# Kernel optimization log

Measured on AMD Instinct MI355X. Metric: run time of the kernel, lower is better.

The kernel has to match this reference:

```python
import jax, jax.numpy as jnp
import numpy as np

EPS = 1e-6

def _elu_feature_map(x):
    # fast_transformers default feature map: elu(x) + 1 (always positive)
    return jax.nn.elu(x) + 1.0

def setup_inputs() -> dict:
    key = jax.random.key(0)
    ks = jax.random.split(key, 7)
    f, n, c, hid = 1024, 64, 256, 1024
    s = 1.0 / np.sqrt(c)
    return {
        "x": jax.random.normal(ks[0], (f, n, c), dtype=jnp.float32),
        "Wq": jax.random.normal(ks[1], (c, hid), dtype=jnp.float32) * s,
        "bq": jax.random.normal(ks[2], (hid,), dtype=jnp.float32) * 0.01,
        "Wk": jax.random.normal(ks[3], (c, hid), dtype=jnp.float32) * s,
        "bk": jax.random.normal(ks[4], (hid,), dtype=jnp.float32) * 0.01,
        "Wv": jax.random.normal(ks[5], (c, hid), dtype=jnp.float32) * s,
        "bv": jax.random.normal(ks[6], (hid,), dtype=jnp.float32) * 0.01,
    }

def reference(x, Wq, bq, Wk, bk, Wv, bv):
    heads = 8
    f, n, c = x.shape
    xt = jnp.transpose(x, (1, 0, 2))  # (n, f, c): joints as batch, frames as sequence
    q = xt @ Wq + bq  # (n, f, hid)
    k = xt @ Wk + bk
    v = xt @ Wv + bv
    hid = q.shape[-1]
    d = hid // heads
    q = q.reshape(n, f, heads, d)
    k = k.reshape(n, f, heads, d)
    v = v.reshape(n, f, heads, d)
    # Linear (kernelized) attention, non-causal (FullMask + full LengthMask)
    Q = _elu_feature_map(q)  # (n, f, h, d)
    K = _elu_feature_map(k)
    KV = jnp.einsum('nshd,nshm->nhmd', K, v)          # (n, h, d_v, d_k)
    Ksum = K.sum(axis=1)                               # (n, h, d_k)
    Z = 1.0 / (jnp.einsum('nlhd,nhd->nlh', Q, Ksum) + EPS)  # (n, f, h)
    out = jnp.einsum('nlhd,nhmd,nlh->nlhm', Q, KV, Z)  # (n, f, h, d_v)
    # faithful to rearrange('f n h c -> n f (h c)') applied to (n, f, h, d):
    # swaps first two axes -> output shape (f, n, h*d)
    out = jnp.transpose(out, (1, 0, 2, 3)).reshape(f, n, hid)
    return out
```

## Files before the change

kernel.cpp:

```cpp
#include <hip/hip_runtime.h>
#include <hip/hip_bf16.h>

#define F 1024
#define N 64
#define C 256
#define HID 1024
#define NH 8
#define D 128

using bf16x8 = __attribute__((ext_vector_type(8))) short;
using u16x8  = __attribute__((ext_vector_type(8))) unsigned short;
using u16x4  = __attribute__((ext_vector_type(4))) unsigned short;
using f32x4  = __attribute__((ext_vector_type(4))) float;

__device__ __forceinline__ unsigned short f2b(float f) {
    union { float f; unsigned u; } v; v.f = f;
    unsigned u = v.u;
    unsigned r = (u + 0x7fffu + ((u >> 16) & 1u)) >> 16;
    return (unsigned short)r;
}
__device__ __forceinline__ float b2f(unsigned short h) {
    union { unsigned u; float f; } v; v.u = ((unsigned)h) << 16;
    return v.f;
}

__device__ __forceinline__ void load_lds16(const unsigned short* g, unsigned short* l) {
    __builtin_amdgcn_global_load_lds(
        (const __attribute__((address_space(1))) void*)g,
        (__attribute__((address_space(3))) void*)l, 16, 0, 0);
}

__global__ void k_conv_x(const float* __restrict__ x, unsigned short* __restrict__ xt) {
    int row = blockIdx.x * 4 + (threadIdx.x >> 6);
    int lane = threadIdx.x & 63;
    int fi = row >> 6, ni = row & 63;
    float4 a = *(const float4*)(x + row * C + lane * 4);
    u16x4 o;
    o[0] = f2b(a.x); o[1] = f2b(a.y); o[2] = f2b(a.z); o[3] = f2b(a.w);
    *(u16x4*)(xt + (ni * F + fi) * C + lane * 4) = o;
}

__global__ void k_conv_w(const float* __restrict__ Wq, const float* __restrict__ Wk,
                         const float* __restrict__ Wv, unsigned short* __restrict__ Wt) {
    int w = blockIdx.z;
    const float* W = (w == 0) ? Wq : ((w == 1) ? Wk : Wv);
    unsigned short* O = Wt + w * (HID * C);
    int n0 = blockIdx.x * 64, k0 = blockIdx.y * 64;
    __shared__ float t[64][65];
    int tx = threadIdx.x & 63, ty = threadIdx.x >> 6;
#pragma unroll
    for (int i = 0; i < 16; i++) {
        int kl = ty + i * 4;
        t[kl][tx] = W[(k0 + kl) * HID + n0 + tx];
    }
    __syncthreads();
#pragma unroll
    for (int i = 0; i < 16; i++) {
        int nl = ty + i * 4;
        O[(n0 + nl) * C + k0 + tx] = f2b(t[tx][nl]);
    }
}

__global__ __launch_bounds__(512, 2) void k_kv_fused(
    const unsigned short* __restrict__ xt, const unsigned short* __restrict__ Wt,
    const float* __restrict__ bk, const float* __restrict__ bv,
    unsigned short* __restrict__ KVb, float* __restrict__ Ksum) {
    __shared__ unsigned short Ks[128 * 128];
    __shared__ unsigned short Vs[128 * 128];
    __shared__ unsigned short Sx[128 * 32];
    __shared__ unsigned short Sw[128 * 32];

    const int ni = blockIdx.x & 63, h = blockIdx.x >> 6;
    const int b = ni * NH + h;
    const int tid = threadIdx.x, lane = tid & 63, w = tid >> 6;
    const int quad = lane >> 4, l15 = lane & 15;
    const int wm2 = w >> 2, wn2 = w & 3;
    const int srow = w * 16 + (lane >> 2);
    const int scol = (lane & 3) * 8;

    const unsigned short* xb  = xt + ni * (F * C);
    const unsigned short* Wkp = Wt + (HID * C) + (h * D) * C;
    const unsigned short* Wvp = Wt + 2 * (HID * C) + (h * D) * C;
    const float* bkp = bk + h * D;
    const float* bvp = bv + h * D;

    f32x4 acc2[4][2];
#pragma unroll
    for (int i = 0; i < 4; i++)
#pragma unroll
        for (int j = 0; j < 2; j++) acc2[i][j] = (f32x4)0.f;
    float ksacc = 0.f;
    const int zd = tid >> 2, zq = tid & 3;

#pragma unroll 1
    for (int ft = 0; ft < 8; ft++) {
        const unsigned short* xrow = xb + (ft * 128) * C;
#pragma unroll 1
        for (int pv = 0; pv < 2; pv++) {
            const unsigned short* Wp = pv ? Wvp : Wkp;
            f32x4 acc[4][2];
#pragma unroll
            for (int i = 0; i < 4; i++)
#pragma unroll
                for (int j = 0; j < 2; j++) acc[i][j] = (f32x4)0.f;
#pragma unroll
            for (int ks = 0; ks < 8; ks++) {
                const int kof = ks * 32;
                load_lds16(xrow + srow * C + kof + scol, Sx + (w * 16) * 32);
                load_lds16(Wp   + srow * C + kof + scol, Sw + (w * 16) * 32);
                __syncthreads();
                bf16x8 af[4], bfr[2];
#pragma unroll
                for (int mb = 0; mb < 4; mb++)
                    af[mb] = *(const bf16x8*)(Sw + (wm2 * 64 + mb * 16 + l15) * 32 + quad * 8);
#pragma unroll
                for (int nb = 0; nb < 2; nb++)
                    bfr[nb] = *(const bf16x8*)(Sx + (wn2 * 32 + nb * 16 + l15) * 32 + quad * 8);
#pragma unroll
                for (int mb = 0; mb < 4; mb++)
#pragma unroll
                    for (int nb = 0; nb < 2; nb++)
                        acc[mb][nb] = __builtin_amdgcn_mfma_f32_16x16x32_bf16(
                            af[mb], bfr[nb], acc[mb][nb], 0, 0, 0);
                __syncthreads();
            }
            const float* bias = pv ? bvp : bkp;
            unsigned short* T = pv ? Vs : Ks;
#pragma unroll
            for (int mb = 0; mb < 4; mb++)
#pragma unroll
                for (int r = 0; r < 4; r++) {
                    int dd = wm2 * 64 + mb * 16 + quad * 4 + r;
                    float bb = bias[dd];
                    char* rowp = (char*)T + dd * 256;
                    int sw = (dd & 7) << 4;
#pragma unroll
                    for (int nb = 0; nb < 2; nb++) {
                        int fi = wn2 * 32 + nb * 16 + l15;
                        float v = acc[mb][nb][r] + bb;
                        if (!pv) v = (v > 0.f) ? (v + 1.f) : __expf(v);
                        *(unsigned short*)(rowp + ((fi * 2) ^ sw)) = f2b(v);
                    }
                }
            __syncthreads();
        }

#pragma unroll
        for (int k0 = 0; k0 < 128; k0 += 32) {
            bf16x8 af[4], bfr[2];
#pragma unroll
            for (int mb = 0; mb < 4; mb++) {
                int m = wm2 * 64 + mb * 16 + l15;
                af[mb] = *(const bf16x8*)((const char*)Vs + m * 256 +
                                          (((k0 + quad * 8) * 2) ^ ((m & 7) << 4)));
            }
#pragma unroll
            for (int nb = 0; nb < 2; nb++) {
                int d = wn2 * 32 + nb * 16 + l15;
                bfr[nb] = *(const bf16x8*)((const char*)Ks + d * 256 +
                                           (((k0 + quad * 8) * 2) ^ ((d & 7) << 4)));
            }
#pragma unroll
            for (int mb = 0; mb < 4; mb++)
#pragma unroll
                for (int nb = 0; nb < 2; nb++)
                    acc2[mb][nb] = __builtin_amdgcn_mfma_f32_16x16x32_bf16(
                        af[mb], bfr[nb], acc2[mb][nb], 0, 0, 0);
        }

        {
            const char* kr = (const char*)Ks + zd * 256;
            int sw = (zd & 7) << 4;
#pragma unroll
            for (int c = 0; c < 4; c++) {
                u16x8 v = *(const u16x8*)(kr + ((zq * 64 + c * 16) ^ sw));
#pragma unroll
                for (int j = 0; j < 8; j++) ksacc += b2f(v[j]);
            }
        }
    }

    unsigned short* KVp = KVb + b * (D * D);
#pragma unroll
    for (int mb = 0; mb < 4; mb++)
#pragma unroll
        for (int r = 0; r < 4; r++) {
            int m = wm2 * 64 + mb * 16 + quad * 4 + r;
#pragma unroll
            for (int nb = 0; nb < 2; nb++) {
                int d = wn2 * 32 + nb * 16 + l15;
                KVp[m * D + d] = f2b(acc2[mb][nb][r]);
            }
        }

    __syncthreads();
    float* sred = (float*)Sx;
    sred[tid] = ksacc;
    __syncthreads();
    if (tid < 128)
        Ksum[b * D + tid] = sred[4 * tid] + sred[4 * tid + 1] +
                            sred[4 * tid + 2] + sred[4 * tid + 3];
}

__global__ __launch_bounds__(256, 3) void k_out_fused(
    const unsigned short* __restrict__ xt, const unsigned short* __restrict__ Wt,
    const float* __restrict__ bq, const unsigned short* __restrict__ KV,
    const float* __restrict__ Ksum, float* __restrict__ out) {
    __shared__ unsigned short Qs[128 * 128];
    __shared__ unsigned short Sx[128 * 32];
    __shared__ unsigned short Sw[128 * 32];
    __shared__ float Kss[128];
    __shared__ float Zs[128];

    const int ni = blockIdx.x & 63, h = blockIdx.x >> 6;
    const int b = ni * NH + h;
    const int l0 = blockIdx.y * 128;
    const int tid = threadIdx.x, lane = tid & 63, w = tid >> 6;
    const int quad = lane >> 4, l15 = lane & 15;
    const int wm = w >> 1, wn = w & 1;
    const int srow = lane >> 2, scol = (lane & 3) * 8;

    if (tid < 128) Kss[tid] = Ksum[b * D + tid];

    const unsigned short* xrow = xt + (ni * F + l0) * C;
    const unsigned short* Wqp = Wt + (h * D) * C;

    f32x4 acc[4][4];
#pragma unroll
    for (int i = 0; i < 4; i++)
#pragma unroll
        for (int j = 0; j < 4; j++) acc[i][j] = (f32x4)0.f;
#pragma unroll
    for (int ks = 0; ks < 8; ks++) {
        const int kof = ks * 32;
        const unsigned short* ga = xrow + (w * 32 + srow) * C + kof + scol;
        const unsigned short* gw = Wqp + (w * 32 + srow) * C + kof + scol;
        load_lds16(ga,          Sx + (w * 32) * 32);
        load_lds16(ga + 16 * C, Sx + (w * 32 + 16) * 32);
        load_lds16(gw,          Sw + (w * 32) * 32);
        load_lds16(gw + 16 * C, Sw + (w * 32 + 16) * 32);
        __syncthreads();
        bf16x8 af[4], bfr[4];
#pragma unroll
        for (int mb = 0; mb < 4; mb++)
            af[mb] = *(const bf16x8*)(Sx + (wm * 64 + mb * 16 + l15) * 32 + quad * 8);
#pragma unroll
        for (int nb = 0; nb < 4; nb++)
            bfr[nb] = *(const bf16x8*)(Sw + (wn * 64 + nb * 16 + l15) * 32 + quad * 8);
#pragma unroll
        for (int mb = 0; mb < 4; mb++)
#pragma unroll
            for (int nb = 0; nb < 4; nb++)
                acc[mb][nb] = __builtin_amdgcn_mfma_f32_16x16x32_bf16(
                    af[mb], bfr[nb], acc[mb][nb], 0, 0, 0);
        __syncthreads();
    }
    {
        float bcol[4];
#pragma unroll
        for (int nb = 0; nb < 4; nb++) bcol[nb] = bq[h * D + wn * 64 + nb * 16 + l15];
#pragma unroll
        for (int mb = 0; mb < 4; mb++)
#pragma unroll
            for (int r = 0; r < 4; r++) {
                int fi = wm * 64 + mb * 16 + quad * 4 + r;
                char* rowp = (char*)Qs + fi * 256;
                int sw = (fi & 7) << 4;
#pragma unroll
                for (int nb = 0; nb < 4; nb++) {
                    int dd = wn * 64 + nb * 16 + l15;
                    float v = acc[mb][nb][r] + bcol[nb];
                    v = (v > 0.f) ? (v + 1.f) : __expf(v);
                    *(unsigned short*)(rowp + ((dd * 2) ^ sw)) = f2b(v);
                }
            }
    }
    __syncthreads();
    if (tid < 128) {
        const char* qr = (const char*)Qs + tid * 256;
        int sw = (tid & 7) << 4;
        float s = 0.f;
#pragma unroll
        for (int c = 0; c < 16; c++) {
            u16x8 v = *(const u16x8*)(qr + ((c * 16) ^ sw));
#pragma unroll
            for (int j = 0; j < 8; j++) s += b2f(v[j]) * Kss[c * 8 + j];
        }
        Zs[tid] = 1.f / (s + 1e-6f);
    }
    __syncthreads();
    const unsigned short* KVp = KV + b * (D * D);
    f32x4 o4[4][4];
#pragma unroll
    for (int i = 0; i < 4; i++)
#pragma unroll
        for (int j = 0; j < 4; j++) o4[i][j] = (f32x4)0.f;
#pragma unroll
    for (int k0 = 0; k0 < 128; k0 += 32) {
        bf16x8 af[4], bfr[4];
#pragma unroll
        for (int mb = 0; mb < 4; mb++) {
            int m = wm * 64 + mb * 16 + l15;
            af[mb] = *(const bf16x8*)(KVp + m * D + k0 + quad * 8);
        }
#pragma unroll
        for (int nb = 0; nb < 4; nb++) {
            int l = wn * 64 + nb * 16 + l15;
            bfr[nb] = *(const bf16x8*)((const char*)Qs + l * 256 +
                                       (((k0 + quad * 8) * 2) ^ ((l & 7) << 4)));
        }
#pragma unroll
        for (int mb = 0; mb < 4; mb++)
#pragma unroll
            for (int nb = 0; nb < 4; nb++)
                o4[mb][nb] = __builtin_amdgcn_mfma_f32_16x16x32_bf16(
                    af[mb], bfr[nb], o4[mb][nb], 0, 0, 0);
    }
#pragma unroll
    for (int nb = 0; nb < 4; nb++) {
        int l = wn * 64 + nb * 16 + l15;
        float z = Zs[l];
        float* op = out + ((l0 + l) * N + ni) * HID + h * D;
#pragma unroll
        for (int mb = 0; mb < 4; mb++) {
            int m0 = wm * 64 + mb * 16 + quad * 4;
            float4 vv;
            vv.x = o4[mb][nb][0] * z;
            vv.y = o4[mb][nb][1] * z;
            vv.z = o4[mb][nb][2] * z;
            vv.w = o4[mb][nb][3] * z;
            *(float4*)(op + m0) = vv;
        }
    }
}

extern "C" void kernel_launch(void* const* d_in, const int* in_sizes, int n_in,
                              void* d_out, int out_size, void* d_ws, size_t ws_size,
                              hipStream_t stream) {
    const float* x  = (const float*)d_in[0];
    const float* Wq = (const float*)d_in[1];
    const float* bq = (const float*)d_in[2];
    const float* Wk = (const float*)d_in[3];
    const float* bk = (const float*)d_in[4];
    const float* Wv = (const float*)d_in[5];
    const float* bv = (const float*)d_in[6];
    float* out = (float*)d_out;
    char* ws = (char*)d_ws;

    unsigned short* xt   = (unsigned short*)(ws);
    unsigned short* Wt   = (unsigned short*)(ws + 33554432);
    unsigned short* KVb  = (unsigned short*)(ws + 35127296);
    float*          Ksum = (float*)(ws + 51904512);

    k_conv_x<<<16384, 256, 0, stream>>>(x, xt);
    k_conv_w<<<dim3(16, 4, 3), 256, 0, stream>>>(Wq, Wk, Wv, Wt);
    k_kv_fused<<<512, 512, 0, stream>>>(xt, Wt, bk, bv, KVb, Ksum);
    k_out_fused<<<dim3(512, 8), 256, 0, stream>>>(xt, Wt, bq, KVb, Ksum, out);
}
```

Before: 584.7 us.

## Double-buffer x tiles in LDS and read weight fragments directly from global

Both fused kernels now double-buffer the activation tile in LDS, prefetching the next k-slice (and across pv/ft boundaries) while MFMAs run on the current one. Weight fragments are no longer staged through LDS but loaded straight from global memory into registers. The per-iteration barrier before compute is removed and launch bounds for the KV kernel are raised to 4 blocks per CU. This trades LDS traffic and barriers for uncoalesced global weight reads that rely on cache hits, and the remaining synchronisation for the buffer swap may be insufficient.

Measured after the change: 804.4 us. 37.6% more time.

```diff
diff --git a/kernel.cpp b/kernel.cpp
--- a/kernel.cpp
+++ b/kernel.cpp
@@ -61,14 +61,13 @@
     }
 }
 
-__global__ __launch_bounds__(512, 2) void k_kv_fused(
+__global__ __launch_bounds__(512, 4) void k_kv_fused(
     const unsigned short* __restrict__ xt, const unsigned short* __restrict__ Wt,
     const float* __restrict__ bk, const float* __restrict__ bv,
     unsigned short* __restrict__ KVb, float* __restrict__ Ksum) {
     __shared__ unsigned short Ks[128 * 128];
     __shared__ unsigned short Vs[128 * 128];
-    __shared__ unsigned short Sx[128 * 32];
-    __shared__ unsigned short Sw[128 * 32];
+    __shared__ unsigned short Sx[2][128 * 32];
 
     const int ni = blockIdx.x & 63, h = blockIdx.x >> 6;
     const int b = ni * NH + h;
@@ -92,6 +91,9 @@
     float ksacc = 0.f;
     const int zd = tid >> 2, zq = tid & 3;
 
+    load_lds16(xb + srow * C + scol, Sx[0] + (w * 16) * 32);
+    __syncthreads();
+
 #pragma unroll 1
     for (int ft = 0; ft < 8; ft++) {
         const unsigned short* xrow = xb + (ft * 128) * C;
@@ -105,17 +107,23 @@
                 for (int j = 0; j < 2; j++) acc[i][j] = (f32x4)0.f;
 #pragma unroll
             for (int ks = 0; ks < 8; ks++) {
-                const int kof = ks * 32;
-                load_lds16(xrow + srow * C + kof + scol, Sx + (w * 16) * 32);
-                load_lds16(Wp   + srow * C + kof + scol, Sw + (w * 16) * 32);
-                __syncthreads();
+                const int cur = ks & 1;
+                if (ks < 7) {
+                    load_lds16(xrow + srow * C + (ks + 1) * 32 + scol,
+                               Sx[cur ^ 1] + (w * 16) * 32);
+                } else if (!(ft == 7 && pv == 1)) {
+                    const unsigned short* nxt = (pv == 0) ? xrow : (xrow + 128 * C);
+                    load_lds16(nxt + srow * C + scol, Sx[cur ^ 1] + (w * 16) * 32);
+                }
                 bf16x8 af[4], bfr[2];
 #pragma unroll
                 for (int mb = 0; mb < 4; mb++)
-                    af[mb] = *(const bf16x8*)(Sw + (wm2 * 64 + mb * 16 + l15) * 32 + quad * 8);
+                    af[mb] = *(const bf16x8*)(Wp + (wm2 * 64 + mb * 16 + l15) * C +
+                                              ks * 32 + quad * 8);
 #pragma unroll
                 for (int nb = 0; nb < 2; nb++)
-                    bfr[nb] = *(const bf16x8*)(Sx + (wn2 * 32 + nb * 16 + l15) * 32 + quad * 8);
+                    bfr[nb] = *(const bf16x8*)(Sx[cur] + (wn2 * 32 + nb * 16 + l15) * 32 +
+                                               quad * 8);
 #pragma unroll
                 for (int mb = 0; mb < 4; mb++)
 #pragma unroll
@@ -194,7 +202,7 @@
         }
 
     __syncthreads();
-    float* sred = (float*)Sx;
+    float* sred = (float*)Sx[0];
     sred[tid] = ksacc;
     __syncthreads();
     if (tid < 128)
@@ -207,8 +215,7 @@
     const float* __restrict__ bq, const unsigned short* __restrict__ KV,
     const float* __restrict__ Ksum, float* __restrict__ out) {
     __shared__ unsigned short Qs[128 * 128];
-    __shared__ unsigned short Sx[128 * 32];
-    __shared__ unsigned short Sw[128 * 32];
+    __shared__ unsigned short Sx[2][128 * 32];
     __shared__ float Kss[128];
     __shared__ float Zs[128];
 
@@ -225,6 +232,10 @@
     const unsigned short* xrow = xt + (ni * F + l0) * C;
     const unsigned short* Wqp = Wt + (h * D) * C;
 
+    load_lds16(xrow + (w * 32 + srow) * C + scol,        Sx[0] + (w * 32) * 32);
+    load_lds16(xrow + (w * 32 + 16 + srow) * C + scol,   Sx[0] + (w * 32 + 16) * 32);
+    __syncthreads();
+
     f32x4 acc[4][4];
 #pragma unroll
     for (int i = 0; i < 4; i++)
@@ -232,21 +243,20 @@
         for (int j = 0; j < 4; j++) acc[i][j] = (f32x4)0.f;
 #pragma unroll
     for (int ks = 0; ks < 8; ks++) {
-        const int kof = ks * 32;
-        const unsigned short* ga = xrow + (w * 32 + srow) * C + kof + scol;
-        const unsigned short* gw = Wqp + (w * 32 + srow) * C + kof + scol;
-        load_lds16(ga,          Sx + (w * 32) * 32);
-        load_lds16(ga + 16 * C, Sx + (w * 32 + 16) * 32);
-        load_lds16(gw,          Sw + (w * 32) * 32);
-        load_lds16(gw + 16 * C, Sw + (w * 32 + 16) * 32);
-        __syncthreads();
+        const int cur = ks & 1;
+        if (ks < 7) {
+            const unsigned short* ga = xrow + (ks + 1) * 32;
+            load_lds16(ga + (w * 32 + srow) * C + scol,      Sx[cur ^ 1] + (w * 32) * 32);
+            load_lds16(ga + (w * 32 + 16 + srow) * C + scol, Sx[cur ^ 1] + (w * 32 + 16) * 32);
+        }
         bf16x8 af[4], bfr[4];
 #pragma unroll
         for (int mb = 0; mb < 4; mb++)
-            af[mb] = *(const bf16x8*)(Sx + (wm * 64 + mb * 16 + l15) * 32 + quad * 8);
+            af[mb] = *(const bf16x8*)(Sx[cur] + (wm * 64 + mb * 16 + l15) * 32 + quad * 8);
 #pragma unroll
         for (int nb = 0; nb < 4; nb++)
-            bfr[nb] = *(const bf16x8*)(Sw + (wn * 64 + nb * 16 + l15) * 32 + quad * 8);
+            bfr[nb] = *(const bf16x8*)(Wqp + (wn * 64 + nb * 16 + l15) * C +
+                                       ks * 32 + quad * 8);
 #pragma unroll
         for (int mb = 0; mb < 4; mb++)
 #pragma unroll
```
